# Performance work log

Hardware: AMD Instinct MI355X
Metric: run time of the kernel (lower is better)

The kernel has to match this reference:

```python
import jax, jax.numpy as jnp
import numpy as np

M_DIM = 256  # attention key dim, used for 1/sqrt(M) scaling


def sparsemax(z):
    # z: [..., F]. Martins & Astudillo sparsemax along last axis.
    F = z.shape[-1]
    zs = -jnp.sort(-z, axis=-1)                      # sorted descending
    css = jnp.cumsum(zs, axis=-1)                    # cumulative sums
    r = jnp.arange(1, F + 1, dtype=z.dtype)
    support = zs * r > (css - 1.0)                   # k(z) condition
    k = jnp.sum(support, axis=-1, keepdims=True)     # support size >= 1
    css_k = jnp.take_along_axis(css, k.astype(jnp.int32) - 1, axis=-1)
    tau = (css_k - 1.0) / k.astype(z.dtype)          # threshold
    return jnp.maximum(z - tau, 0.0)


def setup_inputs() -> dict:
    key = jax.random.key(0)
    ks = jax.random.split(key, 5)
    B, D, F, M = 4096, 1024, 8192, M_DIM
    bound = 0.01
    x = jax.random.normal(ks[0], (B, D), dtype=jnp.float32)
    X_data = jax.random.normal(ks[1], (F, D), dtype=jnp.float32)
    Wq = jax.random.uniform(ks[2], (M, D), dtype=jnp.float32, minval=-bound, maxval=bound)
    Wk = jax.random.uniform(ks[3], (M, D), dtype=jnp.float32, minval=-bound, maxval=bound)
    Wv = jax.random.uniform(ks[4], (D, D), dtype=jnp.float32, minval=-2 * bound, maxval=2 * bound)
    return {
        'x': x, 'X_data': X_data,
        'Wq': Wq, 'bq': jnp.zeros((M,), jnp.float32),
        'Wk': Wk, 'bk': jnp.zeros((M,), jnp.float32),
        'Wv': Wv, 'bv': jnp.zeros((D,), jnp.float32),
    }


def reference(x, X_data, Wq, bq, Wk, bk, Wv, bv):
    M = Wq.shape[0]
    scale = 1.0 / jnp.sqrt(jnp.asarray(M, x.dtype))
    Q = (x @ Wq.T + bq) * scale            # [B, M]
    K = (X_data @ Wk.T + bk) * scale       # [F, M]
    V = X_data @ Wv.T + bv                 # [F, D]
    scores = Q @ K.T                       # [B, F]  (note: 1/M total scaling, as in source)
    attn = sparsemax(scores)               # [B, F], sparse simplex projection
    x_hat = attn @ V                       # [B, D]
    return (x, x_hat, attn)
```

## Files before the change

### kernel.cpp

```cpp
#include <hip/hip_runtime.h>
#include <cstdint>
#include <cstddef>

typedef __attribute__((ext_vector_type(4))) float f32x4;
typedef __attribute__((ext_vector_type(8))) short bf16x8;
typedef __attribute__((ext_vector_type(4))) unsigned short u16x4;
typedef __attribute__((ext_vector_type(8))) unsigned short u16x8;

#define GPTR(p) ((const __attribute__((address_space(1))) void*)(p))
#define LPTR(p) ((__attribute__((address_space(3))) void*)(p))

static constexpr int BB = 4096;
static constexpr int DD = 1024;
static constexpr int FF = 8192;
static constexpr int MM = 256;

__device__ __forceinline__ unsigned short f2bf(float f) {
    union { float f; unsigned u; } x; x.f = f;
    return (unsigned short)((x.u + 0x7FFFu + ((x.u >> 16) & 1u)) >> 16);
}
__device__ __forceinline__ float bf2f(unsigned short h) {
    union { unsigned u; float f; } x; x.u = ((unsigned)h) << 16;
    return x.f;
}
__device__ __forceinline__ int xcd_swz(int bid, int grid) {
    const int cpx = grid >> 3;
    return (bid & 7) * cpx + (bid >> 3);
}

__global__ __launch_bounds__(256) void cvt_bf16(const float* __restrict__ in,
                                                unsigned short* __restrict__ out, int n) {
    int i = (blockIdx.x * 256 + threadIdx.x) * 4;
    if (i >= n) return;
    f32x4 v = *(const f32x4*)(in + i);
    u16x4 o;
    o.x = f2bf(v.x); o.y = f2bf(v.y); o.z = f2bf(v.z); o.w = f2bf(v.w);
    *(u16x4*)(out + i) = o;
}

__global__ __launch_bounds__(256) void cvt_w(
    const float* __restrict__ Wq, const float* __restrict__ Wk, const float* __restrict__ Wv,
    unsigned short* __restrict__ Wqb, unsigned short* __restrict__ Wkb, unsigned short* __restrict__ Wvb)
{
    int i = (blockIdx.x * 256 + threadIdx.x) * 4;
    const float* in; unsigned short* out; int off;
    if (i < MM * DD)            { in = Wq; out = Wqb; off = 0; }
    else if (i < 2 * MM * DD)   { in = Wk; out = Wkb; off = MM * DD; }
    else                        { in = Wv; out = Wvb; off = 2 * MM * DD; }
    const int j = i - off;
    f32x4 v = *(const f32x4*)(in + j);
    u16x4 o;
    o.x = f2bf(v.x); o.y = f2bf(v.y); o.z = f2bf(v.z); o.w = f2bf(v.w);
    *(u16x4*)(out + j) = o;
}

template<int Mo, int No, int Kd, int KC>
__global__ __launch_bounds__(256) void gemm_t(
    const unsigned short* __restrict__ A,
    const unsigned short* __restrict__ Bm,
    unsigned short* __restrict__ P)
{
    constexpr int mt = Mo >> 7, nt = No >> 7;
    constexpr int chunk = Kd / KC;

    __shared__ alignas(16) unsigned short As[128 * 32];
    __shared__ alignas(16) unsigned short Bs[128 * 32];

    const int tid  = threadIdx.x;
    const int lane = tid & 63;
    const int wid  = tid >> 6;
    const int L = xcd_swz(blockIdx.x, KC * mt * nt);
    const int tm = (L % mt) << 7;
    const int r  = L / mt;
    const int tn = (r % nt) << 7;
    const int kc = r / nt;
    const int kbase = kc * chunk;
    const int wm = (wid >> 1) * 64;
    const int wn = (wid & 1) * 64;
    const int lr = lane & 15;
    const int lg = lane >> 4;

    f32x4 acc[4][4] = {};

    const int srow = tid >> 2;
    const int scol = (tid & 3) << 3;
    const unsigned short* aptr = A  + (size_t)(tm + srow) * Kd + kbase + scol;
    const unsigned short* bptr = Bm + (size_t)(tn + srow) * Kd + kbase + scol;
    unsigned short* As_base = &As[wid * 512];
    unsigned short* Bs_base = &Bs[wid * 512];

    for (int k0 = 0; k0 < chunk; k0 += 32) {
        __builtin_amdgcn_global_load_lds(GPTR(aptr + k0),                   LPTR(As_base),        16, 0, 0);
        __builtin_amdgcn_global_load_lds(GPTR(aptr + (size_t)64 * Kd + k0), LPTR(As_base + 2048), 16, 0, 0);
        __builtin_amdgcn_global_load_lds(GPTR(bptr + k0),                   LPTR(Bs_base),        16, 0, 0);
        __builtin_amdgcn_global_load_lds(GPTR(bptr + (size_t)64 * Kd + k0), LPTR(Bs_base + 2048), 16, 0, 0);
        __syncthreads();

        bf16x8 af[4], bfr[4];
        #pragma unroll
        for (int mi = 0; mi < 4; ++mi)
            af[mi] = *(const bf16x8*)&As[(wm + mi * 16 + lr) * 32 + lg * 8];
        #pragma unroll
        for (int ni = 0; ni < 4; ++ni)
            bfr[ni] = *(const bf16x8*)&Bs[(wn + ni * 16 + lr) * 32 + lg * 8];

        #pragma unroll
        for (int mi = 0; mi < 4; ++mi)
            #pragma unroll
            for (int ni = 0; ni < 4; ++ni)
                acc[mi][ni] = __builtin_amdgcn_mfma_f32_16x16x32_bf16(af[mi], bfr[ni], acc[mi][ni], 0, 0, 0);
        __syncthreads();
    }

    unsigned short* Pk = P + (size_t)kc * Mo * No;
    #pragma unroll
    for (int mi = 0; mi < 4; ++mi)
        #pragma unroll
        for (int ni = 0; ni < 4; ++ni)
            #pragma unroll
            for (int r2 = 0; r2 < 4; ++r2) {
                const int row = tm + wm + mi * 16 + lg * 4 + r2;
                const int col = tn + wn + ni * 16 + lr;
                Pk[(size_t)row * No + col] = f2bf(acc[mi][ni][r2]);
            }
}

template<int Mo, int No, int Kd, int KC, int DIRECT>
__global__ __launch_bounds__(512) void gemm256(
    const unsigned short* __restrict__ A,
    const unsigned short* __restrict__ Bm,
    unsigned short* __restrict__ Out)
{
    constexpr int KCH = Kd / KC;
    constexpr int NT  = KCH / 32;
    constexpr int mt  = Mo >> 8;
    constexpr int nt  = No >> 8;

    __shared__ alignas(16) unsigned short SH[4 * 16384];

    const int tid  = threadIdx.x;
    const int lane = tid & 63;
    const int wid  = tid >> 6;
    const int wr   = wid >> 2;
    const int wc   = wid & 3;
    const int lr   = lane & 15;
    const int lg   = lane >> 4;

    const int L  = xcd_swz(blockIdx.x, KC * mt * nt);
    const int tn = (L % nt) << 8;
    const int r0 = L / nt;
    const int tm = (r0 % mt) << 8;
    const int kc = r0 / mt;
    const size_t kbase = (size_t)kc * KCH;

    const unsigned short* ag0 = A  + (size_t)(tm + (tid >> 2)) * Kd + kbase + ((tid & 3) << 3);
    const unsigned short* bg0 = Bm + (size_t)(tn + (tid >> 2)) * Kd + kbase + ((tid & 3) << 3);

    auto STAGE_A = [&](int tt) {
        const int buf = tt & 3;
        #pragma unroll
        for (int s = 0; s < 2; ++s)
            __builtin_amdgcn_global_load_lds(GPTR(ag0 + (size_t)(s * 128) * Kd + tt * 32),
                LPTR(&SH[buf * 16384 + s * 4096 + wid * 512]), 16, 0, 0);
    };
    auto STAGE_B = [&](int tt) {
        const int buf = tt & 3;
        #pragma unroll
        for (int s = 0; s < 2; ++s)
            __builtin_amdgcn_global_load_lds(GPTR(bg0 + (size_t)(s * 128) * Kd + tt * 32),
                LPTR(&SH[buf * 16384 + 8192 + s * 4096 + wid * 512]), 16, 0, 0);
    };

    f32x4 acc[8][4] = {};

    STAGE_A(0); STAGE_B(0);
    STAGE_A(1); STAGE_B(1);
    STAGE_A(2); STAGE_B(2);
    asm volatile("s_waitcnt vmcnt(8)" ::: "memory");
    __builtin_amdgcn_s_barrier();

    #pragma unroll 1
    for (int t = 0; t < NT; ++t) {
        if (t) {
            if (t < NT - 2)      asm volatile("s_waitcnt vmcnt(8)" ::: "memory");
            else if (t == NT-2)  asm volatile("s_waitcnt vmcnt(4)" ::: "memory");
            else                 asm volatile("s_waitcnt vmcnt(0)" ::: "memory");
            __builtin_amdgcn_s_barrier();
        }
        const int buf = t & 3;
        const unsigned short* Ab = &SH[buf * 16384];
        const unsigned short* Bb = &SH[buf * 16384 + 8192];

        bf16x8 bfr[4], af[4];
        #pragma unroll
        for (int ni = 0; ni < 4; ++ni)
            bfr[ni] = *(const bf16x8*)&Bb[(wc * 64 + ni * 16 + lr) * 32 + lg * 8];
        #pragma unroll
        for (int mi = 0; mi < 4; ++mi)
            af[mi] = *(const bf16x8*)&Ab[(wr * 128 + mi * 16 + lr) * 32 + lg * 8];
        if (t + 3 < NT) STAGE_A(t + 3);
        __builtin_amdgcn_sched_barrier(0);
        __builtin_amdgcn_s_setprio(1);
        #pragma unroll
        for (int mi = 0; mi < 4; ++mi)
            #pragma unroll
            for (int ni = 0; ni < 4; ++ni)
                acc[mi][ni] = __builtin_amdgcn_mfma_f32_16x16x32_bf16(af[mi], bfr[ni], acc[mi][ni], 0, 0, 0);
        __builtin_amdgcn_s_setprio(0);
        __builtin_amdgcn_s_barrier();

        bf16x8 af2[4];
        #pragma unroll
        for (int mi = 0; mi < 4; ++mi)
            af2[mi] = *(const bf16x8*)&Ab[(wr * 128 + 64 + mi * 16 + lr) * 32 + lg * 8];
        if (t + 3 < NT) STAGE_B(t + 3);
        __builtin_amdgcn_sched_barrier(0);
        __builtin_amdgcn_s_setprio(1);
        #pragma unroll
        for (int mi = 0; mi < 4; ++mi)
            #pragma unroll
            for (int ni = 0; ni < 4; ++ni)
                acc[4 + mi][ni] = __builtin_amdgcn_mfma_f32_16x16x32_bf16(af2[mi], bfr[ni], acc[4 + mi][ni], 0, 0, 0);
        __builtin_amdgcn_s_setprio(0);
    }

    unsigned short* Ok = DIRECT ? (Out + (size_t)tm * No + tn)
                                : (Out + ((size_t)kc * Mo + tm) * No + tn);
    #pragma unroll
    for (int mi = 0; mi < 8; ++mi)
        #pragma unroll
        for (int ni = 0; ni < 4; ++ni)
            #pragma unroll
            for (int r = 0; r < 4; ++r) {
                const int row = wr * 128 + mi * 16 + lg * 4 + r;
                const int col = wc * 64 + ni * 16 + lr;
                Ok[(size_t)row * No + col] = f2bf(acc[mi][ni][r]);
            }
}

template<int KC, int MODE, int SHIFT = 0>
__global__ __launch_bounds__(256) void reduce_sk(
    const unsigned short* __restrict__ P, void* __restrict__ out,
    const float* __restrict__ bias, size_t total, int NoMask, float scale)
{
    const size_t i = ((size_t)blockIdx.x * 256 + threadIdx.x) * 8;
    float v[8] = {0,0,0,0,0,0,0,0};
    #pragma unroll
    for (int kc = 0; kc < KC; ++kc) {
        u16x8 p = *(const u16x8*)(P + kc * total + i);
        #pragma unroll
        for (int c = 0; c < 8; ++c) v[c] += bf2f(p[c]);
    }
    if (MODE == 1) {
        u16x8 o;
        #pragma unroll
        for (int c = 0; c < 8; ++c)
            o[c] = f2bf((v[c] + bias[(i + c) & NoMask]) * scale);
        *(u16x8*)((unsigned short*)out + i) = o;
    } else if (MODE == 2) {
        const float b = bias[i >> SHIFT];
        u16x8 o;
        #pragma unroll
        for (int c = 0; c < 8; ++c) o[c] = f2bf(v[c] + b);
        *(u16x8*)((unsigned short*)out + i) = o;
    } else {
        f32x4 o0, o1;
        #pragma unroll
        for (int c = 0; c < 4; ++c) { o0[c] = v[c]; o1[c] = v[4 + c]; }
        *(f32x4*)((float*)out + i)     = o0;
        *(f32x4*)((float*)out + i + 4) = o1;
    }
}

__global__ __launch_bounds__(256) void sparsemax_k(unsigned short* __restrict__ SA,
                                                   float* __restrict__ attn)
{
    __shared__ float red[16];
    const int t = threadIdx.x;
    const int w = t >> 6, lane = t & 63;
    unsigned short* Zrow = SA + (size_t)blockIdx.x * FF;
    float* Arow = attn + (size_t)blockIdx.x * FF;

    f32x4 z[8];
    #pragma unroll
    for (int j = 0; j < 4; ++j) {
        u16x8 v = *(const u16x8*)&Zrow[j * 2048 + t * 8];
        #pragma unroll
        for (int c = 0; c < 4; ++c) {
            z[2 * j][c]     = bf2f(v[c]);
            z[2 * j + 1][c] = bf2f(v[4 + c]);
        }
    }

    float mx = -1e30f, sm = 0.0f;
    #pragma unroll
    for (int j = 0; j < 8; ++j)
        #pragma unroll
        for (int c = 0; c < 4; ++c) { mx = fmaxf(mx, z[j][c]); sm += z[j][c]; }
    #pragma unroll
    for (int off = 32; off > 0; off >>= 1) {
        mx = fmaxf(mx, __shfl_xor(mx, off));
        sm += __shfl_xor(sm, off);
    }
    if (lane == 0) { red[w] = mx; red[8 + w] = sm; }
    __syncthreads();
    mx = fmaxf(fmaxf(red[0], red[1]), fmaxf(red[2], red[3]));
    sm = red[8] + red[9] + red[10] + red[11];
    __syncthreads();

    float lo = fmaxf(mx - 1.0f, (sm - 1.0f) * (1.0f / (float)FF));
    float hi = mx - 1.0f / (float)FF;

    for (int it = 0; it < 8; ++it) {
        const float mid = 0.5f * (lo + hi);
        float s = 0.0f;
        #pragma unroll
        for (int j = 0; j < 8; ++j)
            #pragma unroll
            for (int c = 0; c < 4; ++c) s += fmaxf(z[j][c] - mid, 0.0f);
        #pragma unroll
        for (int off = 32; off > 0; off >>= 1) s += __shfl_xor(s, off);
        if (lane == 0) red[w] = s;
        __syncthreads();
        s = red[0] + red[1] + red[2] + red[3];
        __syncthreads();
        if (s >= 1.0f) lo = mid; else hi = mid;
    }

    for (int it = 0; it < 2; ++it) {
        float s = 0.0f, cnt = 0.0f;
        #pragma unroll
        for (int j = 0; j < 8; ++j)
            #pragma unroll
            for (int c = 0; c < 4; ++c) {
                const float v = z[j][c];
                if (v > lo) { s += v; cnt += 1.0f; }
            }
        #pragma unroll
        for (int off = 32; off > 0; off >>= 1) { s += __shfl_xor(s, off); cnt += __shfl_xor(cnt, off); }
        if (lane == 0) { red[w] = s; red[8 + w] = cnt; }
        __syncthreads();
        s   = red[0] + red[1] + red[2] + red[3];
        cnt = red[8] + red[9] + red[10] + red[11];
        __syncthreads();
        lo = (s - 1.0f) / cnt;
    }
    const float tau = lo;

    #pragma unroll
    for (int j = 0; j < 4; ++j) {
        f32x4 a0, a1;
        #pragma unroll
        for (int c = 0; c < 4; ++c) {
            a0[c] = fmaxf(z[2 * j][c] - tau, 0.0f);
            a1[c] = fmaxf(z[2 * j + 1][c] - tau, 0.0f);
        }
        *(f32x4*)&Arow[j * 2048 + t * 8]     = a0;
        *(f32x4*)&Arow[j * 2048 + t * 8 + 4] = a1;
        u16x8 o;
        #pragma unroll
        for (int c = 0; c < 4; ++c) { o[c] = f2bf(a0[c]); o[4 + c] = f2bf(a1[c]); }
        *(u16x8*)&Zrow[j * 2048 + t * 8] = o;
    }
}

extern "C" void kernel_launch(void* const* d_in, const int* in_sizes, int n_in,
                              void* d_out, int out_size, void* d_ws, size_t ws_size,
                              hipStream_t stream) {
    const float* x  = (const float*)d_in[0];
    const float* Xd = (const float*)d_in[1];
    const float* Wq = (const float*)d_in[2];
    const float* bq = (const float*)d_in[3];
    const float* Wk = (const float*)d_in[4];
    const float* bk = (const float*)d_in[5];
    const float* Wv = (const float*)d_in[6];
    const float* bv = (const float*)d_in[7];

    float* out       = (float*)d_out;
    float* out_xhat  = out + (size_t)BB * DD;
    float* out_attn  = out + (size_t)2 * BB * DD;

    char* w = (char*)d_ws;
    unsigned short* xb  = (unsigned short*)w; w += (size_t)BB * DD * 2;
    unsigned short* Xb  = (unsigned short*)w; w += (size_t)FF * DD * 2;
    unsigned short* Wqb = (unsigned short*)w; w += (size_t)MM * DD * 2;
    unsigned short* Wkb = (unsigned short*)w; w += (size_t)MM * DD * 2;
    unsigned short* Wvb = (unsigned short*)w; w += (size_t)DD * DD * 2;
    unsigned short* Qb  = (unsigned short*)w; w += (size_t)BB * MM * 2;
    unsigned short* Kb  = (unsigned short*)w; w += (size_t)FF * MM * 2;
    unsigned short* Vtb = (unsigned short*)w; w += (size_t)DD * FF * 2;
    unsigned short* Sb  = (unsigned short*)w; w += (size_t)BB * FF * 2;

    unsigned short* Pb = (unsigned short*)d_ws;
    unsigned short* PV = Sb;
    unsigned short* PQ = (unsigned short*)out_attn;
    unsigned short* PK = PQ + (size_t)8 * BB * MM;

    hipMemcpyAsync(d_out, d_in[0], (size_t)BB * DD * sizeof(float),
                   hipMemcpyDeviceToDevice, stream);

    cvt_bf16<<<BB * DD / 1024, 256, 0, stream>>>(x,  xb,  BB * DD);
    cvt_bf16<<<FF * DD / 1024, 256, 0, stream>>>(Xd, Xb,  FF * DD);
    cvt_w<<<(2 * MM * DD + DD * DD) / 1024, 256, 0, stream>>>(Wq, Wk, Wv, Wqb, Wkb, Wvb);

    const float scl = 0.0625f;

    gemm_t<BB, MM, DD, 8><<<8 * (BB/128) * (MM/128), 256, 0, stream>>>(xb, Wqb, PQ);
    gemm_t<FF, MM, DD, 4><<<4 * (FF/128) * (MM/128), 256, 0, stream>>>(Xb, Wkb, PK);
    reduce_sk<8, 1><<<BB * MM / 2048, 256, 0, stream>>>(PQ, Qb, bq, (size_t)BB * MM, MM - 1, scl);
    reduce_sk<4, 1><<<FF * MM / 2048, 256, 0, stream>>>(PK, Kb, bk, (size_t)FF * MM, MM - 1, scl);

    gemm256<DD, FF, DD, 2, 0><<<2 * (DD/256) * (FF/256), 512, 0, stream>>>(Wvb, Xb, PV);
    reduce_sk<2, 2, 13><<<DD * FF / 2048, 256, 0, stream>>>(PV, Vtb, bv, (size_t)DD * FF, 0, 1.0f);

    gemm256<BB, FF, MM, 1, 1><<<(BB/256) * (FF/256), 512, 0, stream>>>(Qb, Kb, Sb);

    sparsemax_k<<<BB, 256, 0, stream>>>(Sb, out_attn);

    gemm256<BB, DD, FF, 4, 0><<<4 * (BB/256) * (DD/256), 512, 0, stream>>>(Sb, Vtb, Pb);
    reduce_sk<4, 0><<<BB * DD / 2048, 256, 0, stream>>>(Pb, out_xhat, nullptr, (size_t)BB * DD, 0, 1.0f);
}
```

Measured before the change: 257.3 us.

## Fuse conversions and projection GEMMs into single launches, drop split-K reductions

Merges the three conversion kernels and the x copy into one cvt_all launch that also writes the passthrough output. The Q, K and V projection GEMMs become one proj_all grid of 704 blocks using a 128x128 tile with full K and bias/scale fused into the epilogue. This removes split-K partial buffers, three reduction kernels and several launches. In exchange V now uses the smaller 128 tile instead of the 256 tile, and there is less parallelism per GEMM.

```diff
diff --git a/kernel.cpp b/kernel.cpp
--- a/kernel.cpp
+++ b/kernel.cpp
@@ -28,53 +28,53 @@
     return (bid & 7) * cpx + (bid >> 3);
 }
 
-__global__ __launch_bounds__(256) void cvt_bf16(const float* __restrict__ in,
-                                                unsigned short* __restrict__ out, int n) {
-    int i = (blockIdx.x * 256 + threadIdx.x) * 4;
-    if (i >= n) return;
-    f32x4 v = *(const f32x4*)(in + i);
-    u16x4 o;
-    o.x = f2bf(v.x); o.y = f2bf(v.y); o.z = f2bf(v.z); o.w = f2bf(v.w);
-    *(u16x4*)(out + i) = o;
-}
-
-__global__ __launch_bounds__(256) void cvt_w(
+__global__ __launch_bounds__(256) void cvt_all(
+    const float* __restrict__ x,  const float* __restrict__ Xd,
     const float* __restrict__ Wq, const float* __restrict__ Wk, const float* __restrict__ Wv,
+    float* __restrict__ out_x,
+    unsigned short* __restrict__ xb,  unsigned short* __restrict__ Xb,
     unsigned short* __restrict__ Wqb, unsigned short* __restrict__ Wkb, unsigned short* __restrict__ Wvb)
 {
-    int i = (blockIdx.x * 256 + threadIdx.x) * 4;
-    const float* in; unsigned short* out; int off;
-    if (i < MM * DD)            { in = Wq; out = Wqb; off = 0; }
-    else if (i < 2 * MM * DD)   { in = Wk; out = Wkb; off = MM * DD; }
-    else                        { in = Wv; out = Wvb; off = 2 * MM * DD; }
-    const int j = i - off;
-    f32x4 v = *(const f32x4*)(in + j);
-    u16x4 o;
-    o.x = f2bf(v.x); o.y = f2bf(v.y); o.z = f2bf(v.z); o.w = f2bf(v.w);
-    *(u16x4*)(out + j) = o;
-}
-
-template<int Mo, int No, int Kd, int KC>
-__global__ __launch_bounds__(256) void gemm_t(
+    constexpr int S0 = BB * DD;
+    constexpr int S1 = FF * DD;
+    constexpr int SW = MM * DD;
+    const int i = (blockIdx.x * 256 + threadIdx.x) * 4;
+    if (i < S0) {
+        f32x4 v = *(const f32x4*)(x + i);
+        *(f32x4*)(out_x + i) = v;
+        u16x4 o; o.x = f2bf(v.x); o.y = f2bf(v.y); o.z = f2bf(v.z); o.w = f2bf(v.w);
+        *(u16x4*)(xb + i) = o;
+    } else if (i < S0 + S1) {
+        const int j = i - S0;
+        f32x4 v = *(const f32x4*)(Xd + j);
+        u16x4 o; o.x = f2bf(v.x); o.y = f2bf(v.y); o.z = f2bf(v.z); o.w = f2bf(v.w);
+        *(u16x4*)(Xb + j) = o;
+    } else {
+        int j = i - S0 - S1;
+        const float* in; unsigned short* outp;
+        if (j < SW)            { in = Wq; outp = Wqb; }
+        else if (j < 2 * SW)   { in = Wk; outp = Wkb; j -= SW; }
+        else                   { in = Wv; outp = Wvb; j -= 2 * SW; }
+        f32x4 v = *(const f32x4*)(in + j);
+        u16x4 o; o.x = f2bf(v.x); o.y = f2bf(v.y); o.z = f2bf(v.z); o.w = f2bf(v.w);
+        *(u16x4*)(outp + j) = o;
+    }
+}
+
+template<int Mo, int No, int Kd, int BIAS_MODE>
+__device__ __forceinline__ void gemm128_core(
     const unsigned short* __restrict__ A,
     const unsigned short* __restrict__ Bm,
-    unsigned short* __restrict__ P)
+    unsigned short* __restrict__ Out,
+    const float* __restrict__ bias, float scale,
+    int L, unsigned short* As, unsigned short* Bs)
 {
     constexpr int mt = Mo >> 7, nt = No >> 7;
-    constexpr int chunk = Kd / KC;
-
-    __shared__ alignas(16) unsigned short As[128 * 32];
-    __shared__ alignas(16) unsigned short Bs[128 * 32];
-
     const int tid  = threadIdx.x;
     const int lane = tid & 63;
     const int wid  = tid >> 6;
-    const int L = xcd_swz(blockIdx.x, KC * mt * nt);
     const int tm = (L % mt) << 7;
-    const int r  = L / mt;
-    const int tn = (r % nt) << 7;
-    const int kc = r / nt;
-    const int kbase = kc * chunk;
+    const int tn = ((L / mt) % nt) << 7;
     const int wm = (wid >> 1) * 64;
     const int wn = (wid & 1) * 64;
     const int lr = lane & 15;
@@ -82,14 +82,12 @@
 
     f32x4 acc[4][4] = {};
 
-    const int srow = tid >> 2;
-    const int scol = (tid & 3) << 3;
-    const unsigned short* aptr = A  + (size_t)(tm + srow) * Kd + kbase + scol;
-    const unsigned short* bptr = Bm + (size_t)(tn + srow) * Kd + kbase + scol;
+    const unsigned short* aptr = A  + (size_t)(tm + (tid >> 2)) * Kd + ((tid & 3) << 3);
+    const unsigned short* bptr = Bm + (size_t)(tn + (tid >> 2)) * Kd + ((tid & 3) << 3);
     unsigned short* As_base = &As[wid * 512];
     unsigned short* Bs_base = &Bs[wid * 512];
 
-    for (int k0 = 0; k0 < chunk; k0 += 32) {
+    for (int k0 = 0; k0 < Kd; k0 += 32) {
         __builtin_amdgcn_global_load_lds(GPTR(aptr + k0),                   LPTR(As_base),        16, 0, 0);
         __builtin_amdgcn_global_load_lds(GPTR(aptr + (size_t)64 * Kd + k0), LPTR(As_base + 2048), 16, 0, 0);
         __builtin_amdgcn_global_load_lds(GPTR(bptr + k0),                   LPTR(Bs_base),        16, 0, 0);
@@ -112,17 +110,39 @@
         __syncthreads();
     }
 
-    unsigned short* Pk = P + (size_t)kc * Mo * No;
     #pragma unroll
     for (int mi = 0; mi < 4; ++mi)
         #pragma unroll
         for (int ni = 0; ni < 4; ++ni)
             #pragma unroll
-            for (int r2 = 0; r2 < 4; ++r2) {
-                const int row = tm + wm + mi * 16 + lg * 4 + r2;
+            for (int r = 0; r < 4; ++r) {
+                const int row = tm + wm + mi * 16 + lg * 4 + r;
                 const int col = tn + wn + ni * 16 + lr;
-                Pk[(size_t)row * No + col] = f2bf(acc[mi][ni][r2]);
+                float v = acc[mi][ni][r];
+                if (BIAS_MODE == 1) v = (v + bias[col]) * scale;
+                if (BIAS_MODE == 2) v = v + bias[row];
+                Out[(size_t)row * No + col] = f2bf(v);
             }
+}
+
+__global__ __launch_bounds__(256) void proj_all(
+    const unsigned short* __restrict__ xb,  const unsigned short* __restrict__ Xb,
+    const unsigned short* __restrict__ Wqb, const unsigned short* __restrict__ Wkb,
+    const unsigned short* __restrict__ Wvb,
+    unsigned short* __restrict__ Qb, unsigned short* __restrict__ Kb, unsigned short* __restrict__ Vtb,
+    const float* __restrict__ bq, const float* __restrict__ bk, const float* __restrict__ bv,
+    float scl)
+{
+    __shared__ alignas(16) unsigned short As[128 * 32];
+    __shared__ alignas(16) unsigned short Bs[128 * 32];
+    const int bid = blockIdx.x;
+    if (bid < 512) {
+        gemm128_core<DD, FF, DD, 2>(Wvb, Xb, Vtb, bv, 1.0f, xcd_swz(bid, 512), As, Bs);
+    } else if (bid < 640) {
+        gemm128_core<FF, MM, DD, 1>(Xb, Wkb, Kb, bk, scl, xcd_swz(bid - 512, 128), As, Bs);
+    } else {
+        gemm128_core<BB, MM, DD, 1>(xb, Wqb, Qb, bq, scl, xcd_swz(bid - 640, 64), As, Bs);
+    }
 }
 
 template<int Mo, int No, int Kd, int KC, int DIRECT>
@@ -238,10 +258,9 @@
             }
 }
 
-template<int KC, int MODE, int SHIFT = 0>
+template<int KC>
 __global__ __launch_bounds__(256) void reduce_sk(
-    const unsigned short* __restrict__ P, void* __restrict__ out,
-    const float* __restrict__ bias, size_t total, int NoMask, float scale)
+    const unsigned short* __restrict__ P, float* __restrict__ out, size_t total)
 {
     const size_t i = ((size_t)blockIdx.x * 256 + threadIdx.x) * 8;
     float v[8] = {0,0,0,0,0,0,0,0};
@@ -251,25 +270,11 @@
         #pragma unroll
         for (int c = 0; c < 8; ++c) v[c] += bf2f(p[c]);
     }
-    if (MODE == 1) {
-        u16x8 o;
-        #pragma unroll
-        for (int c = 0; c < 8; ++c)
-            o[c] = f2bf((v[c] + bias[(i + c) & NoMask]) * scale);
-        *(u16x8*)((unsigned short*)out + i) = o;
-    } else if (MODE == 2) {
-        const float b = bias[i >> SHIFT];
-        u16x8 o;
-        #pragma unroll
-        for (int c = 0; c < 8; ++c) o[c] = f2bf(v[c] + b);
-        *(u16x8*)((unsigned short*)out + i) = o;
-    } else {
-        f32x4 o0, o1;
-        #pragma unroll
-        for (int c = 0; c < 4; ++c) { o0[c] = v[c]; o1[c] = v[4 + c]; }
-        *(f32x4*)((float*)out + i)     = o0;
-        *(f32x4*)((float*)out + i + 4) = o1;
-    }
+    f32x4 o0, o1;
+    #pragma unroll
+    for (int c = 0; c < 4; ++c) { o0[c] = v[c]; o1[c] = v[4 + c]; }
+    *(f32x4*)(out + i)     = o0;
+    *(f32x4*)(out + i + 4) = o1;
 }
 
 __global__ __launch_bounds__(256) void sparsemax_k(unsigned short* __restrict__ SA,
@@ -392,31 +397,17 @@
     unsigned short* Sb  = (unsigned short*)w; w += (size_t)BB * FF * 2;
 
     unsigned short* Pb = (unsigned short*)d_ws;
-    unsigned short* PV = Sb;
-    unsigned short* PQ = (unsigned short*)out_attn;
-    unsigned short* PK = PQ + (size_t)8 * BB * MM;
-
-    hipMemcpyAsync(d_out, d_in[0], (size_t)BB * DD * sizeof(float),
-                   hipMemcpyDeviceToDevice, stream);
-
-    cvt_bf16<<<BB * DD / 1024, 256, 0, stream>>>(x,  xb,  BB * DD);
-    cvt_bf16<<<FF * DD / 1024, 256, 0, stream>>>(Xd, Xb,  FF * DD);
-    cvt_w<<<(2 * MM * DD + DD * DD) / 1024, 256, 0, stream>>>(Wq, Wk, Wv, Wqb, Wkb, Wvb);
-
-    const float scl = 0.0625f;
-
-    gemm_t<BB, MM, DD, 8><<<8 * (BB/128) * (MM/128), 256, 0, stream>>>(xb, Wqb, PQ);
-    gemm_t<FF, MM, DD, 4><<<4 * (FF/128) * (MM/128), 256, 0, stream>>>(Xb, Wkb, PK);
-    reduce_sk<8, 1><<<BB * MM / 2048, 256, 0, stream>>>(PQ, Qb, bq, (size_t)BB * MM, MM - 1, scl);
-    reduce_sk<4, 1><<<FF * MM / 2048, 256, 0, stream>>>(PK, Kb, bk, (size_t)FF * MM, MM - 1, scl);
-
-    gemm256<DD, FF, DD, 2, 0><<<2 * (DD/256) * (FF/256), 512, 0, stream>>>(Wvb, Xb, PV);
-    reduce_sk<2, 2, 13><<<DD * FF / 2048, 256, 0, stream>>>(PV, Vtb, bv, (size_t)DD * FF, 0, 1.0f);
+
+    constexpr int CVT_N = BB * DD + FF * DD + 2 * MM * DD + DD * DD;
+    cvt_all<<<CVT_N / 1024, 256, 0, stream>>>(x, Xd, Wq, Wk, Wv, out, xb, Xb, Wqb, Wkb, Wvb);
+
+    proj_all<<<704, 256, 0, stream>>>(xb, Xb, Wqb, Wkb, Wvb, Qb, Kb, Vtb, bq, bk, bv, 0.0625f);
 
     gemm256<BB, FF, MM, 1, 1><<<(BB/256) * (FF/256), 512, 0, stream>>>(Qb, Kb, Sb);
 
     sparsemax_k<<<BB, 256, 0, stream>>>(Sb, out_attn);
 
     gemm256<BB, DD, FF, 4, 0><<<4 * (BB/256) * (DD/256), 512, 0, stream>>>(Sb, Vtb, Pb);
-    reduce_sk<4, 0><<<BB * DD / 2048, 256, 0, stream>>>(Pb, out_xhat, nullptr, (size_t)BB * DD, 0, 1.0f);
-}
+
+    reduce_sk<4><<<BB * DD / 2048, 256, 0, stream>>>(Pb, out_xhat, (size_t)BB * DD);
+}
```

Measured after the change: 214.7 us (median of 2 runs). 1.2x faster.
